# Performance work log

Measured on AMD Instinct MI355X. Metric: run time of the kernel, lower is better.

The kernel has to match this reference:

```python
import jax, jax.numpy as jnp
import numpy as np

B, N, M, DQ, DK, DV, H = 8, 1024, 1024, 512, 512, 512, 8
DH = DV // H           # per-head dim (dim_split)
DFF = 4 * DV           # FFN hidden dim
EPS = 1e-5


def _layernorm(x, g, b):
    mu = jnp.mean(x, axis=-1, keepdims=True)
    var = jnp.mean(jnp.square(x - mu), axis=-1, keepdims=True)
    return (x - mu) * jax.lax.rsqrt(var + EPS) * g + b


def setup_inputs() -> dict:
    key = jax.random.key(0)
    ks = jax.random.split(key, 20)
    s = 0.02
    return {
        "Q": jax.random.normal(ks[0], (B, N, DQ), jnp.float32),
        "K": jax.random.normal(ks[1], (B, M, DK), jnp.float32),
        "Wq": jax.random.normal(ks[2], (DV, DQ), jnp.float32) * s,
        "bq": jnp.zeros((DV,), jnp.float32),
        "Wk": jax.random.normal(ks[3], (DV, DK), jnp.float32) * s,
        "bk": jnp.zeros((DV,), jnp.float32),
        "Wv": jax.random.normal(ks[4], (DV, DK), jnp.float32) * s,
        "bv": jnp.zeros((DV,), jnp.float32),
        "W1": jax.random.normal(ks[5], (DFF, DV), jnp.float32) * s,
        "b1": jnp.zeros((DFF,), jnp.float32),
        "W2": jax.random.normal(ks[6], (DFF, DFF), jnp.float32) * s,
        "b2": jnp.zeros((DFF,), jnp.float32),
        "W3": jax.random.normal(ks[7], (DV, DFF), jnp.float32) * s,
        "b3": jnp.zeros((DV,), jnp.float32),
        "g0": jnp.ones((DV,), jnp.float32),
        "beta0": jnp.zeros((DV,), jnp.float32),
        "g1": jnp.ones((DV,), jnp.float32),
        "beta1": jnp.zeros((DV,), jnp.float32),
    }


def reference(Q, K, Wq, bq, Wk, bk, Wv, bv, W1, b1, W2, b2, W3, b3, g0, beta0, g1, beta1):
    # projections (torch Linear: x @ W.T + b)
    Qp = Q @ Wq.T + bq            # [B, N, DV]
    Kp = K @ Wk.T + bk            # [B, M, DV]
    Vp = K @ Wv.T + bv            # [B, M, DV]

    # split heads: [B, S, DV] -> [B, S, H, DH]
    Qh = Qp.reshape(B, N, H, DH)
    Kh = Kp.reshape(B, M, H, DH)
    Vh = Vp.reshape(B, M, H, DH)

    # scaled dot-product attention (scale = sqrt(head_dim))
    A = jnp.einsum("bnhd,bmhd->bhnm", Qh, Kh) / jnp.sqrt(jnp.float32(DH))
    A = jax.nn.softmax(A, axis=-1)
    O = jnp.einsum("bhnm,bmhd->bnhd", A, Vh).reshape(B, N, DV)

    # residual with projected Q, then LN
    O = _layernorm(O + Qp, g0, beta0)

    # FFN: Linear->ReLU->Linear->ReLU->Linear (num_hidden_layers=2)
    h = jax.nn.relu(O @ W1.T + b1)
    h = jax.nn.relu(h @ W2.T + b2)
    Off = h @ W3.T + b3

    return _layernorm(O + Off, g1, beta1)
```

## Files before the change

### kernel.cpp

```cpp
#include <hip/hip_runtime.h>


typedef __bf16 bf16_t;
typedef __bf16 bf16x8 __attribute__((ext_vector_type(8)));
typedef __bf16 bf16x4 __attribute__((ext_vector_type(4)));
typedef __bf16 bf16x2 __attribute__((ext_vector_type(2)));
typedef float  f32x4  __attribute__((ext_vector_type(4)));
typedef float  f32x16 __attribute__((ext_vector_type(16)));
typedef int    i32x4_t __attribute__((ext_vector_type(4)));
typedef int    i32x8_t __attribute__((ext_vector_type(8)));

__device__ __forceinline__ f32x4 mfma16(bf16x8 a, bf16x8 b, f32x4 c) {
  return __builtin_amdgcn_mfma_f32_16x16x32_bf16(a, b, c, 0, 0, 0);
}

__device__ __forceinline__ void gload_lds16(const void* g, void* l) {
  __builtin_amdgcn_global_load_lds((const __attribute__((address_space(1))) void*)g,
                                   (__attribute__((address_space(3))) void*)l,
                                   16, 0, 0);
}

__device__ __forceinline__ unsigned char to_fp8(float v) {
  return (unsigned char)(__builtin_amdgcn_cvt_pk_fp8_f32(v, v, 0, false) & 0xff);
}

__global__ __launch_bounds__(256) void cast_all(
    const float* __restrict__ Q, const float* __restrict__ K,
    const float* __restrict__ Wq, const float* __restrict__ Wk,
    const float* __restrict__ Wv, const float* __restrict__ W1,
    const float* __restrict__ W2, const float* __restrict__ W3,
    bf16_t* Qb, bf16_t* Kb, bf16_t* Wqb, bf16_t* Wkb, bf16_t* Wvb,
    bf16_t* W1b, unsigned char* W2q, bf16_t* W3b)
{
  long i = ((long)blockIdx.x * 256 + threadIdx.x) * 4;
  if (i >= 10223616L && i < 14417920L) {
    long o = i - 10223616L;
    float4 v = *(const float4*)(W2 + o);
    unsigned int lo = __builtin_amdgcn_cvt_pk_fp8_f32(v.x, v.y, 0, false);
    unsigned int hi = __builtin_amdgcn_cvt_pk_fp8_f32(v.z, v.w, 0, false);
    *(unsigned int*)(W2q + o) = (lo & 0xffffu) | (hi << 16);
    return;
  }
  const float* s; bf16_t* d; long o;
  if      (i <  4194304L) { s = Q;  d = Qb;  o = i;             }
  else if (i <  8388608L) { s = K;  d = Kb;  o = i - 4194304L;  }
  else if (i <  8650752L) { s = Wq; d = Wqb; o = i - 8388608L;  }
  else if (i <  8912896L) { s = Wk; d = Wkb; o = i - 8650752L;  }
  else if (i <  9175040L) { s = Wv; d = Wvb; o = i - 8912896L;  }
  else if (i < 10223616L) { s = W1; d = W1b; o = i - 9175040L;  }
  else                    { s = W3; d = W3b; o = i - 14417920L; }
  float4 v = *(const float4*)(s + o);
  bf16x4 w;
  w[0] = (bf16_t)v.x; w[1] = (bf16_t)v.y; w[2] = (bf16_t)v.z; w[3] = (bf16_t)v.w;
  *(bf16x4*)(d + o) = w;
}

template <int BM, bool RELU, bool VTEPI>
__device__ __forceinline__ void gemm_core(
    const bf16_t* __restrict__ A, const bf16_t* __restrict__ W,
    const float* __restrict__ bias, float* __restrict__ Cf,
    bf16_t* __restrict__ Cb, unsigned char* __restrict__ C8,
    bf16_t* __restrict__ VTout,
    float bscale, int N, int K, int lda, int ldb, int bx, int by)
{
  constexpr int WM = (BM == 128) ? 2 : 1;
  constexpr int WN = 4 / WM;
  constexpr int FI = 4;
  constexpr int FJ = 128 / (WN * 16);
  constexpr int CN = 128 / WN;
  constexpr int AISS = BM / 32;
  constexpr int SM_AB = (BM + 128) * 64 * 2;
  constexpr int SM_TS = 128 * 132 * 2;
  constexpr int SMEM = (VTEPI && SM_TS > SM_AB) ? SM_TS : SM_AB;

  __shared__ __align__(16) char smem[SMEM];
  bf16_t* As = (bf16_t*)smem;
  bf16_t* Bs = (bf16_t*)(smem + BM * 64 * 2);

  const int tid  = threadIdx.x;
  const int wave = tid >> 6, lane = tid & 63;
  const int lq   = lane & 15, quad = lane >> 4;
  const int wm   = (WM == 2) ? (wave & 1) : 0;
  const int wn   = (WM == 2) ? (wave >> 1) : wave;
  const long row0 = (long)bx * BM;
  const long col0 = (long)by * 128;

  const int sr = tid >> 3;
  const int cg = (tid & 7) ^ (sr & 7);
  const bf16_t* ag = A + (row0 + sr) * (long)lda + cg * 8;
  const bf16_t* bg = W + (col0 + sr) * (long)ldb + cg * 8;
  char* asD = (char*)As + wave * 1024;
  char* bsD = (char*)Bs + wave * 1024;

  const int off0 = (quad ^ (lq & 7)) * 8;
  const bf16_t* aR0 = As + (wm * 64 + lq) * 64 + off0;
  const bf16_t* aR1 = As + (wm * 64 + lq) * 64 + (off0 ^ 32);
  const bf16_t* bR0 = Bs + (wn * CN + lq) * 64 + off0;
  const bf16_t* bR1 = Bs + (wn * CN + lq) * 64 + (off0 ^ 32);

  f32x4 acc[FI][FJ];
#pragma unroll
  for (int i = 0; i < FI; i++)
#pragma unroll
    for (int j = 0; j < FJ; j++) acc[i][j] = (f32x4){0.f, 0.f, 0.f, 0.f};

  const long arows32 = 32L * lda;
  const long brows32 = 32L * ldb;
  for (int k0 = 0; k0 < K; k0 += 64) {
    __syncthreads();
#pragma unroll
    for (int is = 0; is < AISS; is++)
      gload_lds16(ag + is * arows32 + k0, asD + is * 4096);
#pragma unroll
    for (int is = 0; is < 4; is++)
      gload_lds16(bg + is * brows32 + k0, bsD + is * 4096);
    __syncthreads();
    bf16x8 af[FI], bw[FJ];
#pragma unroll
    for (int i = 0; i < FI; i++) af[i] = *(const bf16x8*)(aR0 + i * 1024);
#pragma unroll
    for (int j = 0; j < FJ; j++) bw[j] = *(const bf16x8*)(bR0 + j * 1024);
#pragma unroll
    for (int i = 0; i < FI; i++)
#pragma unroll
      for (int j = 0; j < FJ; j++)
        acc[i][j] = mfma16(af[i], bw[j], acc[i][j]);
#pragma unroll
    for (int i = 0; i < FI; i++) af[i] = *(const bf16x8*)(aR1 + i * 1024);
#pragma unroll
    for (int j = 0; j < FJ; j++) bw[j] = *(const bf16x8*)(bR1 + j * 1024);
#pragma unroll
    for (int i = 0; i < FI; i++)
#pragma unroll
      for (int j = 0; j < FJ; j++)
        acc[i][j] = mfma16(af[i], bw[j], acc[i][j]);
  }

  float bc[FJ];
#pragma unroll
  for (int j = 0; j < FJ; j++)
    bc[j] = bias ? bias[col0 + wn * CN + j * 16 + lq] : 0.f;

  if (VTEPI && VTout) {
    bf16_t* Ts = (bf16_t*)smem;
    __syncthreads();
#pragma unroll
    for (int i = 0; i < FI; i++)
#pragma unroll
      for (int j = 0; j < FJ; j++) {
        bf16x4 pv;
#pragma unroll
        for (int r = 0; r < 4; r++) pv[r] = (bf16_t)(acc[i][j][r] + bc[j]);
        *(bf16x4*)(Ts + (wn * CN + j * 16 + lq) * 132 + wm * 64 + i * 16 + quad * 4) = pv;
      }
    __syncthreads();
    const int b  = bx >> 3;
    const int mb = (bx & 7) * 128;
    const int h0 = by * 2;
    const int dd = tid >> 4;
    const int mc = (tid & 15) * 8;
#pragma unroll
    for (int p = 0; p < 8; p++) {
      const int d = dd + p * 16;
      bf16x8 v = *(const bf16x8*)(Ts + d * 132 + mc);
      *(bf16x8*)(VTout + ((long)(b * 8 + h0 + (d >> 6))) * 65536
                 + (d & 63) * 1024 + mb + mc) = v;
    }
    return;
  }

  const long rb = row0 + wm * 64 + quad * 4;
  const long cb = col0 + wn * CN + lq;
#pragma unroll
  for (int i = 0; i < FI; i++)
#pragma unroll
    for (int j = 0; j < FJ; j++)
#pragma unroll
      for (int r = 0; r < 4; r++) {
        float v = acc[i][j][r] + bc[j];
        if (RELU) v = fmaxf(v, 0.f);
        long idx = (rb + i * 16 + r) * (long)N + cb + j * 16;
        if (Cf) Cf[idx] = v;
        if (Cb) Cb[idx] = (bf16_t)(v * bscale);
        if (C8) C8[idx] = to_fp8(v);
      }
}

template <int BM, bool RELU>
__global__ __launch_bounds__(256) void gemm_bt(
    const bf16_t* __restrict__ A, const bf16_t* __restrict__ W,
    const float* __restrict__ bias, float* __restrict__ Cf,
    bf16_t* __restrict__ Cb, unsigned char* __restrict__ C8,
    float bscale, int N, int K)
{
  gemm_core<BM, RELU, false>(A, W, bias, Cf, Cb, C8, nullptr, bscale,
                             N, K, K, K, blockIdx.x, blockIdx.y);
}

__global__ __launch_bounds__(256) void ffn3_splitk(
    const bf16_t* __restrict__ H2, const bf16_t* __restrict__ W3b,
    bf16_t* __restrict__ Off01)
{
  const int z = blockIdx.z;
  gemm_core<128, false, false>(H2 + z * 1024, W3b + z * 1024, nullptr,
                               nullptr, Off01 + (long)z * 4194304, nullptr,
                               nullptr, 1.0f, 512, 1024, 2048, 2048,
                               blockIdx.x, blockIdx.y);
}

__global__ __launch_bounds__(256) void proj3(
    const bf16_t* __restrict__ Qb, const bf16_t* __restrict__ Kb,
    const bf16_t* __restrict__ Wqb, const bf16_t* __restrict__ Wkb,
    const bf16_t* __restrict__ Wvb,
    const float* __restrict__ bq, const float* __restrict__ bk,
    const float* __restrict__ bv,
    bf16_t* Qpb, bf16_t* Kpb, bf16_t* VT)
{
  const int z = blockIdx.z;
  const bf16_t* A  = (z == 0) ? Qb : Kb;
  const bf16_t* Wt = (z == 0) ? Wqb : ((z == 1) ? Wkb : Wvb);
  const float* bias = (z == 0) ? bq : ((z == 1) ? bk : bv);
  bf16_t* Cb = (z == 0) ? Qpb : ((z == 1) ? Kpb : nullptr);
  bf16_t* VTout = (z == 2) ? VT : nullptr;
  const float sc = (z == 1) ? 0.125f : 1.0f;
  gemm_core<128, false, true>(A, Wt, bias, nullptr, Cb, nullptr, VTout, sc,
                              512, 512, 512, 512, blockIdx.x, blockIdx.y);
}

__global__ __launch_bounds__(256) void ffn2_fp8(
    const unsigned char* __restrict__ H1, const unsigned char* __restrict__ W2,
    const float* __restrict__ bias, bf16_t* __restrict__ C)
{
  __shared__ unsigned char As[16384];
  __shared__ unsigned char Bs[16384];
  const int tid = threadIdx.x;
  const int wave = tid >> 6, lane = tid & 63;
  const int wm = wave & 1, wn = wave >> 1;
  const int m = lane & 31, h = lane >> 5;
  const long row0 = (long)blockIdx.x * 128;
  const long col0 = (long)blockIdx.y * 128;

  const int sr = tid >> 3;
  const int cg = (tid & 7) ^ (sr & 7);
  const unsigned char* ag = H1 + (row0 + sr) * 2048 + cg * 16;
  const unsigned char* bg = W2 + (col0 + sr) * 2048 + cg * 16;
  char* asD = (char*)As + wave * 1024;
  char* bsD = (char*)Bs + wave * 1024;

  const int ar0 = wm * 64 + m, ar1 = ar0 + 32;
  const int br0 = wn * 64 + m, br1 = br0 + 32;

  f32x16 acc[2][2];
#pragma unroll
  for (int mi = 0; mi < 2; mi++)
#pragma unroll
    for (int nj = 0; nj < 2; nj++)
#pragma unroll
      for (int r = 0; r < 16; r++) acc[mi][nj][r] = 0.f;

  for (int k0 = 0; k0 < 2048; k0 += 128) {
    __syncthreads();
#pragma unroll
    for (int is = 0; is < 4; is++)
      gload_lds16(ag + is * 65536 + k0, asD + is * 4096);
#pragma unroll
    for (int is = 0; is < 4; is++)
      gload_lds16(bg + is * 65536 + k0, bsD + is * 4096);
    __syncthreads();
#pragma unroll
    for (int ks = 0; ks < 2; ks++) {
      const int c0 = ks * 4 + h * 2;
      i32x8_t a[2], b[2];
#pragma unroll
      for (int mi = 0; mi < 2; mi++) {
        const int r = mi ? ar1 : ar0;
        i32x4_t lo = *(const i32x4_t*)(As + r * 128 + ((c0    ) ^ (r & 7)) * 16);
        i32x4_t hi = *(const i32x4_t*)(As + r * 128 + ((c0 + 1) ^ (r & 7)) * 16);
        a[mi][0] = lo[0]; a[mi][1] = lo[1]; a[mi][2] = lo[2]; a[mi][3] = lo[3];
        a[mi][4] = hi[0]; a[mi][5] = hi[1]; a[mi][6] = hi[2]; a[mi][7] = hi[3];
      }
#pragma unroll
      for (int nj = 0; nj < 2; nj++) {
        const int r = nj ? br1 : br0;
        i32x4_t lo = *(const i32x4_t*)(Bs + r * 128 + ((c0    ) ^ (r & 7)) * 16);
        i32x4_t hi = *(const i32x4_t*)(Bs + r * 128 + ((c0 + 1) ^ (r & 7)) * 16);
        b[nj][0] = lo[0]; b[nj][1] = lo[1]; b[nj][2] = lo[2]; b[nj][3] = lo[3];
        b[nj][4] = hi[0]; b[nj][5] = hi[1]; b[nj][6] = hi[2]; b[nj][7] = hi[3];
      }
#pragma unroll
      for (int mi = 0; mi < 2; mi++)
#pragma unroll
        for (int nj = 0; nj < 2; nj++)
          acc[mi][nj] = __builtin_amdgcn_mfma_scale_f32_32x32x64_f8f6f4(
              a[mi], b[nj], acc[mi][nj], 0, 0,
              0, 0x7f7f7f7f, 0, 0x7f7f7f7f);
    }
  }

  float bc[2];
  bc[0] = bias[col0 + wn * 64 + m];
  bc[1] = bias[col0 + wn * 64 + 32 + m];
#pragma unroll
  for (int mi = 0; mi < 2; mi++)
#pragma unroll
    for (int nj = 0; nj < 2; nj++)
#pragma unroll
      for (int reg = 0; reg < 16; reg++) {
        const int rl = (reg & 3) + 8 * (reg >> 2) + 4 * h;
        float v = fmaxf(acc[mi][nj][reg] + bc[nj], 0.f);
        C[(row0 + wm * 64 + mi * 32 + rl) * 2048 + col0 + wn * 64 + nj * 32 + m]
            = (bf16_t)v;
      }
}

__global__ __launch_bounds__(256) void attn(
    const bf16_t* __restrict__ Qp, const bf16_t* __restrict__ Kp,
    const bf16_t* __restrict__ VT, bf16_t* __restrict__ O)
{
  const int d0 = blockIdx.x;
  const int j  = d0 >> 3;
  const int g  = (d0 & 7) * 8 + (j >> 3);
  const int qb = j & 7;
  const int h  = g & 7, b = g >> 3;

  const int tid = threadIdx.x;
  const int wave = tid >> 6, lane = tid & 63;
  const int lq = lane & 15, quad = lane >> 4;

  __shared__ bf16_t Ks[2][8192];
  __shared__ bf16_t VTs[2][8192];
  __shared__ bf16_t Ps[4][16 * 72];

  const long bh = (long)b * 1024;
  const int qrowA = qb * 128 + wave * 16 + lq;
  const int qrowB = qrowA + 64;

  const bf16_t* qpA = Qp + (bh + qrowA) * 512 + h * 64 + quad * 8;
  const bf16_t* qpB = Qp + (bh + qrowB) * 512 + h * 64 + quad * 8;
  const bf16x8 qfA0 = *(const bf16x8*)qpA;
  const bf16x8 qfA1 = *(const bf16x8*)(qpA + 32);
  const bf16x8 qfB0 = *(const bf16x8*)qpB;
  const bf16x8 qfB1 = *(const bf16x8*)(qpB + 32);

  f32x4 oaccA[4], oaccB[4];
#pragma unroll
  for (int t = 0; t < 4; t++) {
    oaccA[t] = (f32x4){0.f, 0.f, 0.f, 0.f};
    oaccB[t] = (f32x4){0.f, 0.f, 0.f, 0.f};
  }
  float lA = 0.f, lB = 0.f;

  const int sr = tid >> 3;
  const int cg = (tid & 7) ^ (sr & 7);
  const bf16_t* kg  = Kp + bh * 512 + h * 64;
  const bf16_t* vtg = VT + ((long)b * 8 + h) * 65536;
  const int off0 = (quad ^ (lq & 7)) * 8;

  auto stage = [&](int m0, int bi) {
    char* ksDst = (char*)(Ks[bi]) + wave * 1024;
    char* vtDst = (char*)(VTs[bi]) + wave * 1024;
#pragma unroll
    for (int s = 0; s < 2; s++) {
      gload_lds16(kg + (long)(m0 + s * 64 + sr) * 512 + cg * 8,      ksDst + s * 8192);
      gload_lds16(kg + (long)(m0 + s * 64 + sr + 32) * 512 + cg * 8, ksDst + s * 8192 + 4096);
      gload_lds16(vtg + (long)sr * 1024 + m0 + s * 64 + cg * 8,        vtDst + s * 8192);
      gload_lds16(vtg + (long)(sr + 32) * 1024 + m0 + s * 64 + cg * 8, vtDst + s * 8192 + 4096);
    }
  };

  stage(0, 0);

  for (int t = 0; t < 8; ++t) {
    const int cur = t & 1;
    if (t < 7) {
      stage((t + 1) * 128, cur ^ 1);
      asm volatile("s_waitcnt vmcnt(8)" ::: "memory");
    } else {
      asm volatile("s_waitcnt vmcnt(0)" ::: "memory");
    }
    __builtin_amdgcn_s_barrier();
    __builtin_amdgcn_sched_barrier(0);

    const bf16_t* Kc = Ks[cur];
    const bf16_t* Vc = VTs[cur];

    f32x4 stA[8], stB[8];
#pragma unroll
    for (int tt = 0; tt < 8; tt++) {
      const bf16_t* kb = Kc + (tt >> 2) * 4096 + ((tt & 3) * 16 + lq) * 64;
      bf16x8 ka0 = *(const bf16x8*)(kb + off0);
      bf16x8 ka1 = *(const bf16x8*)(kb + (off0 ^ 32));
      f32x4 sA = (f32x4){0.f, 0.f, 0.f, 0.f};
      sA = mfma16(ka0, qfA0, sA);
      sA = mfma16(ka1, qfA1, sA);
      stA[tt] = sA;
      f32x4 sB = (f32x4){0.f, 0.f, 0.f, 0.f};
      sB = mfma16(ka0, qfB0, sB);
      sB = mfma16(ka1, qfB1, sB);
      stB[tt] = sB;
    }

    float lsA = 0.f, lsB = 0.f;
#pragma unroll
    for (int tt = 0; tt < 8; tt++)
#pragma unroll
      for (int r = 0; r < 4; r++) {
        float pA = __expf(stA[tt][r]);
        stA[tt][r] = pA;
        lsA += pA;
        float pB = __expf(stB[tt][r]);
        stB[tt][r] = pB;
        lsB += pB;
      }
    lsA += __shfl_xor(lsA, 16, 64);
    lsA += __shfl_xor(lsA, 32, 64);
    lA += lsA;
    lsB += __shfl_xor(lsB, 16, 64);
    lsB += __shfl_xor(lsB, 32, 64);
    lB += lsB;

    bf16_t* pw = &Ps[wave][0];
#pragma unroll
    for (int hh = 0; hh < 2; hh++) {
#pragma unroll
      for (int tt = 0; tt < 4; tt++) {
        bf16x4 pv;
#pragma unroll
        for (int r = 0; r < 4; r++) pv[r] = (bf16_t)stA[hh * 4 + tt][r];
        *(bf16x4*)(pw + lq * 72 + tt * 16 + quad * 4) = pv;
      }
#pragma unroll
      for (int ks = 0; ks < 2; ks++) {
        bf16x8 pb = *(const bf16x8*)(pw + lq * 72 + ks * 32 + quad * 8);
#pragma unroll
        for (int dt = 0; dt < 4; dt++) {
          const bf16_t* vb = Vc + hh * 4096 + (dt * 16 + lq) * 64;
          bf16x8 va = *(const bf16x8*)(vb + (ks ? (off0 ^ 32) : off0));
          oaccA[dt] = mfma16(va, pb, oaccA[dt]);
        }
      }
    }
#pragma unroll
    for (int hh = 0; hh < 2; hh++) {
#pragma unroll
      for (int tt = 0; tt < 4; tt++) {
        bf16x4 pv;
#pragma unroll
        for (int r = 0; r < 4; r++) pv[r] = (bf16_t)stB[hh * 4 + tt][r];
        *(bf16x4*)(pw + lq * 72 + tt * 16 + quad * 4) = pv;
      }
#pragma unroll
      for (int ks = 0; ks < 2; ks++) {
        bf16x8 pb = *(const bf16x8*)(pw + lq * 72 + ks * 32 + quad * 8);
#pragma unroll
        for (int dt = 0; dt < 4; dt++) {
          const bf16_t* vb = Vc + hh * 4096 + (dt * 16 + lq) * 64;
          bf16x8 va = *(const bf16x8*)(vb + (ks ? (off0 ^ 32) : off0));
          oaccB[dt] = mfma16(va, pb, oaccB[dt]);
        }
      }
    }

    __builtin_amdgcn_sched_barrier(0);
    __builtin_amdgcn_s_barrier();
  }

  const float invA = 1.f / lA;
  const float invB = 1.f / lB;
  bf16_t* opA = O + (bh + qrowA) * 512 + h * 64 + quad * 4;
  bf16_t* opB = O + (bh + qrowB) * 512 + h * 64 + quad * 4;
#pragma unroll
  for (int dt = 0; dt < 4; dt++) {
    bf16x4 vA, vB;
#pragma unroll
    for (int r = 0; r < 4; r++) {
      vA[r] = (bf16_t)(oaccA[dt][r] * invA);
      vB[r] = (bf16_t)(oaccB[dt][r] * invB);
    }
    *(bf16x4*)(opA + dt * 16) = vA;
    *(bf16x4*)(opB + dt * 16) = vB;
  }
}

__device__ __forceinline__ float2 ld2(const float* p, long row, int tid) {
  return ((const float2*)(p + row * 512))[tid];
}
__device__ __forceinline__ float2 ld2(const bf16_t* p, long row, int tid) {
  bf16x2 v = *(const bf16x2*)(p + row * 512 + tid * 2);
  return make_float2((float)v[0], (float)v[1]);
}

__device__ __forceinline__ void ln_finish(
    float x0, float x1, const float* g, const float* be, int tid,
    int wave, int lane, float* of, bf16_t* ob, long row)
{
  float s = x0 + x1, ss = x0 * x0 + x1 * x1;
#pragma unroll
  for (int off = 1; off < 64; off <<= 1) {
    s  += __shfl_xor(s,  off, 64);
    ss += __shfl_xor(ss, off, 64);
  }
  __shared__ float sm[8];
  if (lane == 0) { sm[wave] = s; sm[4 + wave] = ss; }
  __syncthreads();
  s  = sm[0] + sm[1] + sm[2] + sm[3];
  ss = sm[4] + sm[5] + sm[6] + sm[7];
  const float mu = s * (1.f / 512.f);
  const float var = ss * (1.f / 512.f) - mu * mu;
  const float rs = rsqrtf(var + 1e-5f);
  const float2 gg = ((const float2*)g)[tid];
  const float2 bb = ((const float2*)be)[tid];
  const float o0 = (x0 - mu) * rs * gg.x + bb.x;
  const float o1 = (x1 - mu) * rs * gg.y + bb.y;
  if (of) ((float2*)(of + row * 512))[tid] = make_float2(o0, o1);
  if (ob) {
    bf16x2 t; t[0] = (bf16_t)o0; t[1] = (bf16_t)o1;
    *(bf16x2*)(ob + row * 512 + tid * 2) = t;
  }
}

__global__ __launch_bounds__(256) void ln_res(
    const bf16_t* __restrict__ A, const bf16_t* __restrict__ Bv,
    const float* __restrict__ g, const float* __restrict__ be,
    bf16_t* __restrict__ ob)
{
  const int row = blockIdx.x, tid = threadIdx.x;
  const float2 va = ld2(A,  (long)row, tid);
  const float2 vb = ld2(Bv, (long)row, tid);
  ln_finish(va.x + vb.x, va.y + vb.y, g, be, tid, tid >> 6, tid & 63,
            nullptr, ob, row);
}

__global__ __launch_bounds__(256) void ln_res3(
    const bf16_t* __restrict__ X, const bf16_t* __restrict__ O0,
    const bf16_t* __restrict__ O1, const float* __restrict__ bias,
    const float* __restrict__ g, const float* __restrict__ be,
    float* __restrict__ of)
{
  const int row = blockIdx.x, tid = threadIdx.x;
  const float2 vx = ld2(X,  (long)row, tid);
  const float2 v0 = ld2(O0, (long)row, tid);
  const float2 v1 = ld2(O1, (long)row, tid);
  const float2 vb = ((const float2*)bias)[tid];
  ln_finish(vx.x + v0.x + v1.x + vb.x, vx.y + v0.y + v1.y + vb.y,
            g, be, tid, tid >> 6, tid & 63, of, nullptr, row);
}

extern "C" void kernel_launch(void* const* d_in, const int* in_sizes, int n_in,
                              void* d_out, int out_size, void* d_ws, size_t ws_size,
                              hipStream_t stream)
{
  const float* Q   = (const float*)d_in[0];
  const float* K   = (const float*)d_in[1];
  const float* Wq  = (const float*)d_in[2];
  const float* bq  = (const float*)d_in[3];
  const float* Wk  = (const float*)d_in[4];
  const float* bk  = (const float*)d_in[5];
  const float* Wv  = (const float*)d_in[6];
  const float* bv  = (const float*)d_in[7];
  const float* W1  = (const float*)d_in[8];
  const float* b1  = (const float*)d_in[9];
  const float* W2  = (const float*)d_in[10];
  const float* b2  = (const float*)d_in[11];
  const float* W3  = (const float*)d_in[12];
  const float* b3  = (const float*)d_in[13];
  const float* g0  = (const float*)d_in[14];
  const float* be0 = (const float*)d_in[15];
  const float* g1  = (const float*)d_in[16];
  const float* be1 = (const float*)d_in[17];

  char* ws = (char*)d_ws;
  bf16_t* Wqb = (bf16_t*)(ws + 0);
  bf16_t* Wkb = (bf16_t*)(ws + 524288);
  bf16_t* Wvb = (bf16_t*)(ws + 1048576);
  bf16_t* W1b = (bf16_t*)(ws + 1572864);
  bf16_t* W3b = (bf16_t*)(ws + 3670016);
  unsigned char* W2q = (unsigned char*)(ws + 5767168);
  bf16_t* Qb  = (bf16_t*)(ws + 14155776);
  bf16_t* Kb  = (bf16_t*)(ws + 22544384);
  bf16_t* Qpb = (bf16_t*)(ws + 30932992);
  bf16_t* Kpb = (bf16_t*)(ws + 39321600);
  bf16_t* VT  = (bf16_t*)(ws + 47710208);
  bf16_t* Of  = (bf16_t*)(ws + 14155776);
  bf16_t* Xb  = (bf16_t*)(ws + 22544384);
  bf16_t* H2  = (bf16_t*)(ws + 30932992);
  unsigned char* H1q = (unsigned char*)(ws + 64487424);
  bf16_t* Off0 = (bf16_t*)(ws + 64487424);
  bf16_t* Off1 = (bf16_t*)(ws + 72876032);
  float*  out = (float*)d_out;

  cast_all<<<15104, 256, 0, stream>>>(Q, K, Wq, Wk, Wv, W1, W2, W3,
                                      Qb, Kb, Wqb, Wkb, Wvb, W1b, W2q, W3b);
  proj3<<<dim3(64, 4, 3), 256, 0, stream>>>(Qb, Kb, Wqb, Wkb, Wvb, bq, bk, bv,
                                            Qpb, Kpb, VT);
  attn<<<dim3(512, 1, 1), 256, 0, stream>>>(Qpb, Kpb, VT, Of);
  ln_res<<<8192, 256, 0, stream>>>(Of, Qpb, g0, be0, Xb);
  gemm_bt<128, true ><<<dim3(64, 16), 256, 0, stream>>>(Xb, W1b, b1, nullptr, nullptr, H1q, 1.0f, 2048, 512);
  ffn2_fp8<<<dim3(64, 16), 256, 0, stream>>>(H1q, W2q, b2, H2);
  ffn3_splitk<<<dim3(64, 4, 2), 256, 0, stream>>>(H2, W3b, Off0);
  ln_res3<<<8192, 256, 0, stream>>>(Xb, Off0, Off1, b3, g1, be1, out);
}
```

Measured before the change: 268.4 us.

## Double-buffer LDS tiles in GEMM kernels and swizzle block order for L2 reuse

The shared bf16 GEMM core and the fp8 FFN2 kernel now keep two LDS stages. Each iteration issues the next tile's global-to-LDS loads before computing on the current tile, using explicit vmcnt waits and raw barriers so load latency overlaps with MFMA work. The FFN1 and FFN2 launches move to a 1D grid, with a remap that groups row blocks in 8x8 tiles to improve L2 reuse of the A and W tiles. The trade-off is twice the LDS per block (64KB), which can cut the number of resident blocks per CU, and more reliance on hand-placed wait counts.

```diff
diff --git a/kernel.cpp b/kernel.cpp
--- a/kernel.cpp
+++ b/kernel.cpp
@@ -63,25 +63,21 @@
     bf16_t* __restrict__ VTout,
     float bscale, int N, int K, int lda, int ldb, int bx, int by)
 {
-  constexpr int WM = (BM == 128) ? 2 : 1;
-  constexpr int WN = 4 / WM;
+  static_assert(BM == 128, "gemm_core tuned for BM=128");
   constexpr int FI = 4;
-  constexpr int FJ = 128 / (WN * 16);
-  constexpr int CN = 128 / WN;
-  constexpr int AISS = BM / 32;
-  constexpr int SM_AB = (BM + 128) * 64 * 2;
-  constexpr int SM_TS = 128 * 132 * 2;
-  constexpr int SMEM = (VTEPI && SM_TS > SM_AB) ? SM_TS : SM_AB;
+  constexpr int FJ = 4;
+  constexpr int CN = 64;
+  constexpr int AISS = 4;
+  constexpr int SM_HALF = (BM + 128) * 64 * 2;
+  constexpr int SMEM = 2 * SM_HALF;
 
   __shared__ __align__(16) char smem[SMEM];
-  bf16_t* As = (bf16_t*)smem;
-  bf16_t* Bs = (bf16_t*)(smem + BM * 64 * 2);
 
   const int tid  = threadIdx.x;
   const int wave = tid >> 6, lane = tid & 63;
   const int lq   = lane & 15, quad = lane >> 4;
-  const int wm   = (WM == 2) ? (wave & 1) : 0;
-  const int wn   = (WM == 2) ? (wave >> 1) : wave;
+  const int wm   = wave & 1;
+  const int wn   = wave >> 1;
   const long row0 = (long)bx * BM;
   const long col0 = (long)by * 128;
 
@@ -89,51 +85,69 @@
   const int cg = (tid & 7) ^ (sr & 7);
   const bf16_t* ag = A + (row0 + sr) * (long)lda + cg * 8;
   const bf16_t* bg = W + (col0 + sr) * (long)ldb + cg * 8;
-  char* asD = (char*)As + wave * 1024;
-  char* bsD = (char*)Bs + wave * 1024;
-
-  const int off0 = (quad ^ (lq & 7)) * 8;
-  const bf16_t* aR0 = As + (wm * 64 + lq) * 64 + off0;
-  const bf16_t* aR1 = As + (wm * 64 + lq) * 64 + (off0 ^ 32);
-  const bf16_t* bR0 = Bs + (wn * CN + lq) * 64 + off0;
-  const bf16_t* bR1 = Bs + (wn * CN + lq) * 64 + (off0 ^ 32);
-
-  f32x4 acc[FI][FJ];
-#pragma unroll
-  for (int i = 0; i < FI; i++)
-#pragma unroll
-    for (int j = 0; j < FJ; j++) acc[i][j] = (f32x4){0.f, 0.f, 0.f, 0.f};
-
+  const int asOff = wave * 1024;
+  const int bsOff = BM * 128 + wave * 1024;
   const long arows32 = 32L * lda;
   const long brows32 = 32L * ldb;
-  for (int k0 = 0; k0 < K; k0 += 64) {
-    __syncthreads();
+
+  auto stage = [&](int k0, int bi) {
+    char* base = smem + bi * SM_HALF;
 #pragma unroll
     for (int is = 0; is < AISS; is++)
-      gload_lds16(ag + is * arows32 + k0, asD + is * 4096);
+      gload_lds16(ag + is * arows32 + k0, base + asOff + is * 4096);
 #pragma unroll
     for (int is = 0; is < 4; is++)
-      gload_lds16(bg + is * brows32 + k0, bsD + is * 4096);
-    __syncthreads();
+      gload_lds16(bg + is * brows32 + k0, base + bsOff + is * 4096);
+  };
+
+  const int off0 = (quad ^ (lq & 7)) * 8;
+  const int aO0 = ((wm * 64 + lq) * 64 + off0) * 2;
+  const int aO1 = ((wm * 64 + lq) * 64 + (off0 ^ 32)) * 2;
+  const int bO0 = BM * 128 + ((wn * CN + lq) * 64 + off0) * 2;
+  const int bO1 = BM * 128 + ((wn * CN + lq) * 64 + (off0 ^ 32)) * 2;
+
+  f32x4 acc[FI][FJ];
+#pragma unroll
+  for (int i = 0; i < FI; i++)
+#pragma unroll
+    for (int j = 0; j < FJ; j++) acc[i][j] = (f32x4){0.f, 0.f, 0.f, 0.f};
+
+  stage(0, 0);
+  const int nt = K >> 6;
+  for (int t = 0; t < nt; ++t) {
+    const int cur = t & 1;
+    if (t < nt - 1) {
+      stage((t + 1) * 64, cur ^ 1);
+      asm volatile("s_waitcnt vmcnt(8)" ::: "memory");
+    } else {
+      asm volatile("s_waitcnt vmcnt(0)" ::: "memory");
+    }
+    __builtin_amdgcn_s_barrier();
+    __builtin_amdgcn_sched_barrier(0);
+
+    const char* base = smem + cur * SM_HALF;
     bf16x8 af[FI], bw[FJ];
 #pragma unroll
-    for (int i = 0; i < FI; i++) af[i] = *(const bf16x8*)(aR0 + i * 1024);
-#pragma unroll
-    for (int j = 0; j < FJ; j++) bw[j] = *(const bf16x8*)(bR0 + j * 1024);
+    for (int i = 0; i < FI; i++) af[i] = *(const bf16x8*)(base + aO0 + i * 2048);
+#pragma unroll
+    for (int j = 0; j < FJ; j++) bw[j] = *(const bf16x8*)(base + bO0 + j * 2048);
 #pragma unroll
     for (int i = 0; i < FI; i++)
 #pragma unroll
       for (int j = 0; j < FJ; j++)
         acc[i][j] = mfma16(af[i], bw[j], acc[i][j]);
 #pragma unroll
-    for (int i = 0; i < FI; i++) af[i] = *(const bf16x8*)(aR1 + i * 1024);
-#pragma unroll
-    for (int j = 0; j < FJ; j++) bw[j] = *(const bf16x8*)(bR1 + j * 1024);
+    for (int i = 0; i < FI; i++) af[i] = *(const bf16x8*)(base + aO1 + i * 2048);
+#pragma unroll
+    for (int j = 0; j < FJ; j++) bw[j] = *(const bf16x8*)(base + bO1 + j * 2048);
 #pragma unroll
     for (int i = 0; i < FI; i++)
 #pragma unroll
       for (int j = 0; j < FJ; j++)
         acc[i][j] = mfma16(af[i], bw[j], acc[i][j]);
+
+    __builtin_amdgcn_sched_barrier(0);
+    __builtin_amdgcn_s_barrier();
   }
 
   float bc[FJ];
@@ -193,8 +207,11 @@
     bf16_t* __restrict__ Cb, unsigned char* __restrict__ C8,
     float bscale, int N, int K)
 {
+  const int d  = blockIdx.x;
+  const int bx = (d & 7) * 8 + ((d >> 3) & 7);
+  const int by = d >> 6;
   gemm_core<BM, RELU, false>(A, W, bias, Cf, Cb, C8, nullptr, bscale,
-                             N, K, K, K, blockIdx.x, blockIdx.y);
+                             N, K, K, K, bx, by);
 }
 
 __global__ __launch_bounds__(256) void ffn3_splitk(
@@ -231,42 +248,59 @@
     const unsigned char* __restrict__ H1, const unsigned char* __restrict__ W2,
     const float* __restrict__ bias, bf16_t* __restrict__ C)
 {
-  __shared__ unsigned char As[16384];
-  __shared__ unsigned char Bs[16384];
+  __shared__ unsigned char As[2][16384];
+  __shared__ unsigned char Bs[2][16384];
   const int tid = threadIdx.x;
   const int wave = tid >> 6, lane = tid & 63;
   const int wm = wave & 1, wn = wave >> 1;
   const int m = lane & 31, h = lane >> 5;
-  const long row0 = (long)blockIdx.x * 128;
-  const long col0 = (long)blockIdx.y * 128;
+  const int d  = blockIdx.x;
+  const int bxi = (d & 7) * 8 + ((d >> 3) & 7);
+  const int byi = d >> 6;
+  const long row0 = (long)bxi * 128;
+  const long col0 = (long)byi * 128;
 
   const int sr = tid >> 3;
   const int cg = (tid & 7) ^ (sr & 7);
   const unsigned char* ag = H1 + (row0 + sr) * 2048 + cg * 16;
   const unsigned char* bg = W2 + (col0 + sr) * 2048 + cg * 16;
-  char* asD = (char*)As + wave * 1024;
-  char* bsD = (char*)Bs + wave * 1024;
-
-  const int ar0 = wm * 64 + m, ar1 = ar0 + 32;
-  const int br0 = wn * 64 + m, br1 = br0 + 32;
-
-  f32x16 acc[2][2];
-#pragma unroll
-  for (int mi = 0; mi < 2; mi++)
-#pragma unroll
-    for (int nj = 0; nj < 2; nj++)
-#pragma unroll
-      for (int r = 0; r < 16; r++) acc[mi][nj][r] = 0.f;
-
-  for (int k0 = 0; k0 < 2048; k0 += 128) {
-    __syncthreads();
+
+  auto stage = [&](int k0, int bi) {
+    char* asD = (char*)As[bi] + wave * 1024;
+    char* bsD = (char*)Bs[bi] + wave * 1024;
 #pragma unroll
     for (int is = 0; is < 4; is++)
       gload_lds16(ag + is * 65536 + k0, asD + is * 4096);
 #pragma unroll
     for (int is = 0; is < 4; is++)
       gload_lds16(bg + is * 65536 + k0, bsD + is * 4096);
-    __syncthreads();
+  };
+
+  const int ar0 = wm * 64 + m, ar1 = ar0 + 32;
+  const int br0 = wn * 64 + m, br1 = wn * 64 + 32 + m;
+
+  f32x16 acc[2][2];
+#pragma unroll
+  for (int mi = 0; mi < 2; mi++)
+#pragma unroll
+    for (int nj = 0; nj < 2; nj++)
+#pragma unroll
+      for (int r = 0; r < 16; r++) acc[mi][nj][r] = 0.f;
+
+  stage(0, 0);
+  for (int t = 0; t < 16; ++t) {
+    const int cur = t & 1;
+    if (t < 15) {
+      stage((t + 1) * 128, cur ^ 1);
+      asm volatile("s_waitcnt vmcnt(8)" ::: "memory");
+    } else {
+      asm volatile("s_waitcnt vmcnt(0)" ::: "memory");
+    }
+    __builtin_amdgcn_s_barrier();
+    __builtin_amdgcn_sched_barrier(0);
+
+    const unsigned char* Ac = As[cur];
+    const unsigned char* Bc = Bs[cur];
 #pragma unroll
     for (int ks = 0; ks < 2; ks++) {
       const int c0 = ks * 4 + h * 2;
@@ -274,16 +308,16 @@
 #pragma unroll
       for (int mi = 0; mi < 2; mi++) {
         const int r = mi ? ar1 : ar0;
-        i32x4_t lo = *(const i32x4_t*)(As + r * 128 + ((c0    ) ^ (r & 7)) * 16);
-        i32x4_t hi = *(const i32x4_t*)(As + r * 128 + ((c0 + 1) ^ (r & 7)) * 16);
+        i32x4_t lo = *(const i32x4_t*)(Ac + r * 128 + ((c0    ) ^ (r & 7)) * 16);
+        i32x4_t hi = *(const i32x4_t*)(Ac + r * 128 + ((c0 + 1) ^ (r & 7)) * 16);
         a[mi][0] = lo[0]; a[mi][1] = lo[1]; a[mi][2] = lo[2]; a[mi][3] = lo[3];
         a[mi][4] = hi[0]; a[mi][5] = hi[1]; a[mi][6] = hi[2]; a[mi][7] = hi[3];
       }
 #pragma unroll
       for (int nj = 0; nj < 2; nj++) {
         const int r = nj ? br1 : br0;
-        i32x4_t lo = *(const i32x4_t*)(Bs + r * 128 + ((c0    ) ^ (r & 7)) * 16);
-        i32x4_t hi = *(const i32x4_t*)(Bs + r * 128 + ((c0 + 1) ^ (r & 7)) * 16);
+        i32x4_t lo = *(const i32x4_t*)(Bc + r * 128 + ((c0    ) ^ (r & 7)) * 16);
+        i32x4_t hi = *(const i32x4_t*)(Bc + r * 128 + ((c0 + 1) ^ (r & 7)) * 16);
         b[nj][0] = lo[0]; b[nj][1] = lo[1]; b[nj][2] = lo[2]; b[nj][3] = lo[3];
         b[nj][4] = hi[0]; b[nj][5] = hi[1]; b[nj][6] = hi[2]; b[nj][7] = hi[3];
       }
@@ -295,6 +329,9 @@
               a[mi], b[nj], acc[mi][nj], 0, 0,
               0, 0x7f7f7f7f, 0, 0x7f7f7f7f);
     }
+
+    __builtin_amdgcn_sched_barrier(0);
+    __builtin_amdgcn_s_barrier();
   }
 
   float bc[2];
@@ -595,8 +632,8 @@
                                             Qpb, Kpb, VT);
   attn<<<dim3(512, 1, 1), 256, 0, stream>>>(Qpb, Kpb, VT, Of);
   ln_res<<<8192, 256, 0, stream>>>(Of, Qpb, g0, be0, Xb);
-  gemm_bt<128, true ><<<dim3(64, 16), 256, 0, stream>>>(Xb, W1b, b1, nullptr, nullptr, H1q, 1.0f, 2048, 512);
-  ffn2_fp8<<<dim3(64, 16), 256, 0, stream>>>(H1q, W2q, b2, H2);
+  gemm_bt<128, true ><<<dim3(1024, 1, 1), 256, 0, stream>>>(Xb, W1b, b1, nullptr, nullptr, H1q, 1.0f, 2048, 512);
+  ffn2_fp8<<<dim3(1024, 1, 1), 256, 0, stream>>>(H1q, W2q, b2, H2);
   ffn3_splitk<<<dim3(64, 4, 2), 256, 0, stream>>>(H2, W3b, Off0);
   ln_res3<<<8192, 256, 0, stream>>>(Xb, Off0, Off1, b3, g1, be1, out);
 }
```

New measurement: 271.4 us. No clear change (+1.1%).

## Double-buffer LDS tiles in bf16 GEMM core with async prefetch

Applied to the files above, without the earlier changes.

The bf16 GEMM core now uses a K-step of 32 with two LDS buffers. It prefetches the next tile via global_load_lds while computing on the current one, syncing with explicit vmcnt waits and raw s_barrier instead of two __syncthreads per iteration. The BM template parameter is removed, the tile is fixed at 128x128 and the LDS swizzle is adapted to 64-byte rows. The aim is to hide global load latency behind MFMA work, at the cost of twice as many loop iterations and barriers per K.

```diff
diff --git a/kernel.cpp b/kernel.cpp
--- a/kernel.cpp
+++ b/kernel.cpp
@@ -55,7 +55,7 @@
   *(bf16x4*)(d + o) = w;
 }
 
-template <int BM, bool RELU, bool VTEPI>
+template <bool RELU, bool VTEPI>
 __device__ __forceinline__ void gemm_core(
     const bf16_t* __restrict__ A, const bf16_t* __restrict__ W,
     const float* __restrict__ bias, float* __restrict__ Cf,
@@ -63,40 +63,41 @@
     bf16_t* __restrict__ VTout,
     float bscale, int N, int K, int lda, int ldb, int bx, int by)
 {
-  constexpr int WM = (BM == 128) ? 2 : 1;
-  constexpr int WN = 4 / WM;
   constexpr int FI = 4;
-  constexpr int FJ = 128 / (WN * 16);
-  constexpr int CN = 128 / WN;
-  constexpr int AISS = BM / 32;
-  constexpr int SM_AB = (BM + 128) * 64 * 2;
-  constexpr int SM_TS = 128 * 132 * 2;
-  constexpr int SMEM = (VTEPI && SM_TS > SM_AB) ? SM_TS : SM_AB;
+  constexpr int FJ = 4;
+  constexpr int SM_HALF = 16384;
+  constexpr int SMEM = VTEPI ? (128 * 132 * 2) : 2 * SM_HALF;
+  static_assert(!VTEPI || 128 * 132 * 2 >= 2 * SM_HALF, "Ts covers dbuf");
 
   __shared__ __align__(16) char smem[SMEM];
-  bf16_t* As = (bf16_t*)smem;
-  bf16_t* Bs = (bf16_t*)(smem + BM * 64 * 2);
 
   const int tid  = threadIdx.x;
   const int wave = tid >> 6, lane = tid & 63;
   const int lq   = lane & 15, quad = lane >> 4;
-  const int wm   = (WM == 2) ? (wave & 1) : 0;
-  const int wn   = (WM == 2) ? (wave >> 1) : wave;
-  const long row0 = (long)bx * BM;
+  const int wm   = wave & 1;
+  const int wn   = wave >> 1;
+  const long row0 = (long)bx * 128;
   const long col0 = (long)by * 128;
 
-  const int sr = tid >> 3;
-  const int cg = (tid & 7) ^ (sr & 7);
-  const bf16_t* ag = A + (row0 + sr) * (long)lda + cg * 8;
-  const bf16_t* bg = W + (col0 + sr) * (long)ldb + cg * 8;
-  char* asD = (char*)As + wave * 1024;
-  char* bsD = (char*)Bs + wave * 1024;
-
-  const int off0 = (quad ^ (lq & 7)) * 8;
-  const bf16_t* aR0 = As + (wm * 64 + lq) * 64 + off0;
-  const bf16_t* aR1 = As + (wm * 64 + lq) * 64 + (off0 ^ 32);
-  const bf16_t* bR0 = Bs + (wn * CN + lq) * 64 + off0;
-  const bf16_t* bR1 = Bs + (wn * CN + lq) * 64 + (off0 ^ 32);
+  const int srS = tid >> 2;
+  const int cgS = ((tid & 3) ^ (srS & 3) ^ ((srS >> 2) & 3)) * 8;
+  const bf16_t* agS = A + (row0 + srS) * (long)lda + cgS;
+  const bf16_t* bgS = W + (col0 + srS) * (long)ldb + cgS;
+  const int dstO = wave * 1024;
+  const long arows64 = 64L * lda;
+  const long brows64 = 64L * ldb;
+
+  auto stage = [&](int k0, int bi) {
+    char* base = smem + bi * SM_HALF;
+    gload_lds16(agS + k0,           base +         dstO);
+    gload_lds16(agS + arows64 + k0, base +  4096 + dstO);
+    gload_lds16(bgS + k0,           base +  8192 + dstO);
+    gload_lds16(bgS + brows64 + k0, base + 12288 + dstO);
+  };
+
+  const int so = (quad ^ (lq & 3) ^ ((lq >> 2) & 3)) * 16;
+  const int aB = (wm * 64 + lq) * 64 + so;
+  const int bB = 8192 + (wn * 64 + lq) * 64 + so;
 
   f32x4 acc[FI][FJ];
 #pragma unroll
@@ -104,42 +105,39 @@
 #pragma unroll
     for (int j = 0; j < FJ; j++) acc[i][j] = (f32x4){0.f, 0.f, 0.f, 0.f};
 
-  const long arows32 = 32L * lda;
-  const long brows32 = 32L * ldb;
-  for (int k0 = 0; k0 < K; k0 += 64) {
-    __syncthreads();
-#pragma unroll
-    for (int is = 0; is < AISS; is++)
-      gload_lds16(ag + is * arows32 + k0, asD + is * 4096);
-#pragma unroll
-    for (int is = 0; is < 4; is++)
-      gload_lds16(bg + is * brows32 + k0, bsD + is * 4096);
-    __syncthreads();
+  const int nt = K >> 5;
+  stage(0, 0);
+  for (int t = 0; t < nt; ++t) {
+    const int cur = t & 1;
+    if (t < nt - 1) {
+      stage((t + 1) * 32, cur ^ 1);
+      asm volatile("s_waitcnt vmcnt(4)" ::: "memory");
+    } else {
+      asm volatile("s_waitcnt vmcnt(0)" ::: "memory");
+    }
+    __builtin_amdgcn_s_barrier();
+    __builtin_amdgcn_sched_barrier(0);
+
+    const char* base = smem + cur * SM_HALF;
     bf16x8 af[FI], bw[FJ];
 #pragma unroll
-    for (int i = 0; i < FI; i++) af[i] = *(const bf16x8*)(aR0 + i * 1024);
-#pragma unroll
-    for (int j = 0; j < FJ; j++) bw[j] = *(const bf16x8*)(bR0 + j * 1024);
+    for (int i = 0; i < FI; i++) af[i] = *(const bf16x8*)(base + aB + i * 1024);
+#pragma unroll
+    for (int j = 0; j < FJ; j++) bw[j] = *(const bf16x8*)(base + bB + j * 1024);
 #pragma unroll
     for (int i = 0; i < FI; i++)
 #pragma unroll
       for (int j = 0; j < FJ; j++)
         acc[i][j] = mfma16(af[i], bw[j], acc[i][j]);
-#pragma unroll
-    for (int i = 0; i < FI; i++) af[i] = *(const bf16x8*)(aR1 + i * 1024);
-#pragma unroll
-    for (int j = 0; j < FJ; j++) bw[j] = *(const bf16x8*)(bR1 + j * 1024);
-#pragma unroll
-    for (int i = 0; i < FI; i++)
-#pragma unroll
-      for (int j = 0; j < FJ; j++)
-        acc[i][j] = mfma16(af[i], bw[j], acc[i][j]);
+
+    __builtin_amdgcn_sched_barrier(0);
+    __builtin_amdgcn_s_barrier();
   }
 
   float bc[FJ];
 #pragma unroll
   for (int j = 0; j < FJ; j++)
-    bc[j] = bias ? bias[col0 + wn * CN + j * 16 + lq] : 0.f;
+    bc[j] = bias ? bias[col0 + wn * 64 + j * 16 + lq] : 0.f;
 
   if (VTEPI && VTout) {
     bf16_t* Ts = (bf16_t*)smem;
@@ -151,7 +149,7 @@
         bf16x4 pv;
 #pragma unroll
         for (int r = 0; r < 4; r++) pv[r] = (bf16_t)(acc[i][j][r] + bc[j]);
-        *(bf16x4*)(Ts + (wn * CN + j * 16 + lq) * 132 + wm * 64 + i * 16 + quad * 4) = pv;
+        *(bf16x4*)(Ts + (wn * 64 + j * 16 + lq) * 132 + wm * 64 + i * 16 + quad * 4) = pv;
       }
     __syncthreads();
     const int b  = bx >> 3;
@@ -170,7 +168,7 @@
   }
 
   const long rb = row0 + wm * 64 + quad * 4;
-  const long cb = col0 + wn * CN + lq;
+  const long cb = col0 + wn * 64 + lq;
 #pragma unroll
   for (int i = 0; i < FI; i++)
 #pragma unroll
@@ -186,15 +184,15 @@
       }
 }
 
-template <int BM, bool RELU>
+template <bool RELU>
 __global__ __launch_bounds__(256) void gemm_bt(
     const bf16_t* __restrict__ A, const bf16_t* __restrict__ W,
     const float* __restrict__ bias, float* __restrict__ Cf,
     bf16_t* __restrict__ Cb, unsigned char* __restrict__ C8,
     float bscale, int N, int K)
 {
-  gemm_core<BM, RELU, false>(A, W, bias, Cf, Cb, C8, nullptr, bscale,
-                             N, K, K, K, blockIdx.x, blockIdx.y);
+  gemm_core<RELU, false>(A, W, bias, Cf, Cb, C8, nullptr, bscale,
+                         N, K, K, K, blockIdx.x, blockIdx.y);
 }
 
 __global__ __launch_bounds__(256) void ffn3_splitk(
@@ -202,10 +200,10 @@
     bf16_t* __restrict__ Off01)
 {
   const int z = blockIdx.z;
-  gemm_core<128, false, false>(H2 + z * 1024, W3b + z * 1024, nullptr,
-                               nullptr, Off01 + (long)z * 4194304, nullptr,
-                               nullptr, 1.0f, 512, 1024, 2048, 2048,
-                               blockIdx.x, blockIdx.y);
+  gemm_core<false, false>(H2 + z * 1024, W3b + z * 1024, nullptr,
+                          nullptr, Off01 + (long)z * 4194304, nullptr,
+                          nullptr, 1.0f, 512, 1024, 2048, 2048,
+                          blockIdx.x, blockIdx.y);
 }
 
 __global__ __launch_bounds__(256) void proj3(
@@ -223,8 +221,8 @@
   bf16_t* Cb = (z == 0) ? Qpb : ((z == 1) ? Kpb : nullptr);
   bf16_t* VTout = (z == 2) ? VT : nullptr;
   const float sc = (z == 1) ? 0.125f : 1.0f;
-  gemm_core<128, false, true>(A, Wt, bias, nullptr, Cb, nullptr, VTout, sc,
-                              512, 512, 512, 512, blockIdx.x, blockIdx.y);
+  gemm_core<false, true>(A, Wt, bias, nullptr, Cb, nullptr, VTout, sc,
+                         512, 512, 512, 512, blockIdx.x, blockIdx.y);
 }
 
 __global__ __launch_bounds__(256) void ffn2_fp8(
@@ -248,7 +246,7 @@
   char* bsD = (char*)Bs + wave * 1024;
 
   const int ar0 = wm * 64 + m, ar1 = ar0 + 32;
-  const int br0 = wn * 64 + m, br1 = br0 + 32;
+  const int br0 = wn * 64 + m, br1 = wn * 64 + 32 + m;
 
   f32x16 acc[2][2];
 #pragma unroll
@@ -595,7 +593,7 @@
                                             Qpb, Kpb, VT);
   attn<<<dim3(512, 1, 1), 256, 0, stream>>>(Qpb, Kpb, VT, Of);
   ln_res<<<8192, 256, 0, stream>>>(Of, Qpb, g0, be0, Xb);
-  gemm_bt<128, true ><<<dim3(64, 16), 256, 0, stream>>>(Xb, W1b, b1, nullptr, nullptr, H1q, 1.0f, 2048, 512);
+  gemm_bt<true ><<<dim3(64, 16), 256, 0, stream>>>(Xb, W1b, b1, nullptr, nullptr, H1q, 1.0f, 2048, 512);
   ffn2_fp8<<<dim3(64, 16), 256, 0, stream>>>(H1q, W2q, b2, H2);
   ffn3_splitk<<<dim3(64, 4, 2), 256, 0, stream>>>(H2, W3b, Off0);
   ln_res3<<<8192, 256, 0, stream>>>(Xb, Off0, Off1, b3, g1, be1, out);
```

Measured after the change: 289.3 us. +7.8%, slower.
